# Performance work log

Hardware: AMD Instinct MI355X
Metric: run time of the kernel (lower is better)

Reference implementation:

```python
import jax, jax.numpy as jnp
import numpy as np

N_E = 1024
E_DIM = 256
BETA = 0.25
N = 131072


def setup_inputs() -> dict:
    key = jax.random.key(0)
    k1, k2 = jax.random.split(key)
    z = jax.random.normal(k1, (N, E_DIM), dtype=jnp.float32)
    # original init: uniform(-1/n_e, 1/n_e)
    emb_weight = jax.random.uniform(k2, (N_E, E_DIM), dtype=jnp.float32,
                                    minval=-1.0 / N_E, maxval=1.0 / N_E)
    return {"z": z, "emb_weight": emb_weight}


def reference(z, emb_weight):
    # pairwise squared distances: ||z||^2 + ||e||^2 - 2 z @ e^T   -> [N, n_e]
    d = (jnp.sum(z * z, axis=1, keepdims=True)
         + jnp.sum(emb_weight * emb_weight, axis=1)
         - 2.0 * jnp.matmul(z, emb_weight.T))
    min_encoding_indices = jnp.argmin(d, axis=1)            # [N]
    z_q = emb_weight[min_encoding_indices]                  # gather == one-hot matmul
    sg = jax.lax.stop_gradient
    loss = (jnp.mean((sg(z_q) - z) ** 2)
            + BETA * jnp.mean((z_q - sg(z)) ** 2))
    z_q_st = z + sg(z_q - z)                                # straight-through
    return z_q_st, loss, min_encoding_indices[:, None]
```

## Files before the change

kernel.cpp:

```cpp
#include <hip/hip_runtime.h>
#include <cfloat>

#define NROWS 131072
#define EDIM 256
#define NE 1024
#define DELTA 2.0e-4f

#define BM 128
#define BN 128
#define BK 32

typedef unsigned short u16;
typedef __attribute__((ext_vector_type(8))) short bf16x8;
typedef __attribute__((ext_vector_type(4))) float f32x4;

#define WS_Z2    0u
#define WS_E2    524288u
#define WS_PART  528384u
#define WS_CNT   548864u
#define WS_LIST  549120u
#define WS_CI1   1073408u
#define WS_CI2   1597696u
#define WS_FLG   2121984u
#define WS_BP    2646272u
#define WS_END   4219136u

__device__ __forceinline__ float np_sumsq256(const float* __restrict__ row) {
    float s[2];
#pragma unroll
    for (int h = 0; h < 2; ++h) {
        const float* a = row + h * 128;
        float r[8];
#pragma unroll
        for (int j = 0; j < 8; ++j) r[j] = __fmul_rn(a[j], a[j]);
        for (int i = 8; i < 128; i += 8) {
#pragma unroll
            for (int j = 0; j < 8; ++j)
                r[j] = __fadd_rn(r[j], __fmul_rn(a[i + j], a[i + j]));
        }
        s[h] = __fadd_rn(__fadd_rn(__fadd_rn(r[0], r[1]), __fadd_rn(r[2], r[3])),
                         __fadd_rn(__fadd_rn(r[4], r[5]), __fadd_rn(r[6], r[7])));
    }
    return __fadd_rn(s[0], s[1]);
}

__device__ __forceinline__ u16 bf16_rn(float x) {
    unsigned u = __float_as_uint(x);
    return (u16)((u + 0x7fffu + ((u >> 16) & 1u)) >> 16);
}

__global__ __launch_bounds__(256)
void rownorm_split_kernel(const float* __restrict__ z, float* __restrict__ z2out,
                          u16* __restrict__ zhi, u16* __restrict__ zlo) {
    __shared__ float zl[16 * 256];
    const int tid = threadIdx.x;
    const size_t base4 = (size_t)blockIdx.x * 1024;

    {
        const float4* src = reinterpret_cast<const float4*>(z) + base4;
        float4* dst = reinterpret_cast<float4*>(zl);
#pragma unroll
        for (int i = 0; i < 4; ++i) dst[tid + 256 * i] = src[tid + 256 * i];
    }
    __syncthreads();

    {
        const int row = tid >> 4;
        const int j16 = tid & 15;
        const int h = j16 >> 3, j = j16 & 7;
        const float* a = &zl[row * 256 + h * 128];
        float r = __fmul_rn(a[j], a[j]);
#pragma unroll
        for (int i = 8; i < 128; i += 8)
            r = __fadd_rn(r, __fmul_rn(a[i + j], a[i + j]));
        r = __fadd_rn(r, __shfl_xor(r, 1));
        r = __fadd_rn(r, __shfl_xor(r, 2));
        r = __fadd_rn(r, __shfl_xor(r, 4));
        r = __fadd_rn(r, __shfl_xor(r, 8));
        if (j16 == 0) z2out[blockIdx.x * 16 + row] = r;
    }

    {
        ushort4* ph = reinterpret_cast<ushort4*>(zhi) + base4;
        ushort4* pl = reinterpret_cast<ushort4*>(zlo) + base4;
        const float4* sp = reinterpret_cast<const float4*>(zl);
#pragma unroll
        for (int i = 0; i < 4; ++i) {
            const int q = tid + 256 * i;
            float4 v = sp[q];
            float xs[4] = {v.x, v.y, v.z, v.w};
            u16 hh[4], lo[4];
#pragma unroll
            for (int c = 0; c < 4; ++c) {
                u16 hv = bf16_rn(xs[c]);
                float hf = __uint_as_float(((unsigned)hv) << 16);
                hh[c] = hv;
                lo[c] = bf16_rn(__fsub_rn(xs[c], hf));
            }
            ph[q] = make_ushort4(hh[0], hh[1], hh[2], hh[3]);
            pl[q] = make_ushort4(lo[0], lo[1], lo[2], lo[3]);
        }
    }
}

__global__ __launch_bounds__(256)
void rownorm_kernel(const float* __restrict__ x, float* __restrict__ out, int nrows) {
    int row = blockIdx.x * blockDim.x + threadIdx.x;
    if (row < nrows) out[row] = np_sumsq256(x + (size_t)row * EDIM);
}

__global__ __launch_bounds__(256)
void build_b_kernel(const float* __restrict__ e, u16* __restrict__ Bp) {
    int idx = blockIdx.x * 256 + threadIdx.x;
    int row = idx >> 8, k = idx & 255;
    float x = e[idx];
    u16 hh = bf16_rn(x);
    float hf = __uint_as_float(((unsigned)hh) << 16);
    u16 lo = bf16_rn(__fsub_rn(x, hf));
    Bp[row * 768 + k] = hh;
    Bp[row * 768 + 256 + k] = hh;
    Bp[row * 768 + 512 + k] = lo;
}

__device__ __forceinline__ void gload_lds16(const void* g, void* lds) {
    __builtin_amdgcn_global_load_lds((const __attribute__((address_space(1))) void*)g,
                                     (__attribute__((address_space(3))) void*)lds,
                                     16, 0, 0);
}

#define LEXLT(va, ia, vb, ib) ((va) < (vb) || ((va) == (vb) && (ia) < (ib)))

#define MERGE5(a1, ai1, a2, ai2, a3, b1, bi1, b2, bi2, b3)                    \
    {                                                                         \
        float n1v, n2v, n3v; int n1i, n2i;                                    \
        if (LEXLT(a1, ai1, b1, bi1)) {                                        \
            n1v = a1; n1i = ai1;                                              \
            if (LEXLT(a2, ai2, b1, bi1)) { n2v = a2; n2i = ai2; n3v = fminf(a3, b1); } \
            else                          { n2v = b1; n2i = bi1; n3v = fminf(a2, b2); } \
        } else {                                                              \
            n1v = b1; n1i = bi1;                                              \
            if (LEXLT(b2, bi2, a1, ai1)) { n2v = b2; n2i = bi2; n3v = fminf(b3, a1); } \
            else                          { n2v = a1; n2i = ai1; n3v = fminf(b2, a2); } \
        }                                                                     \
        a1 = n1v; ai1 = n1i; a2 = n2v; ai2 = n2i; a3 = n3v;                   \
    }

__global__ __launch_bounds__(256, 3)
void vq_mfma_kernel(const u16* __restrict__ zhi, const u16* __restrict__ zlo,
                    const u16* __restrict__ Bp, const float* __restrict__ e2f,
                    int* __restrict__ ci1, int* __restrict__ ci2, int* __restrict__ cflag) {
    __shared__ __align__(16) u16  At[128 * 64];
    __shared__ __align__(16) u16  Bt[128 * 64];
    __shared__ float e2s[1024];
    __shared__ float mrg[128 * 2 * 4];

    const int tid = threadIdx.x;
    const int m0  = blockIdx.x * 128;
    const int l   = tid & 63;
    const int wid = tid >> 6;
    const int wrg = wid >> 1;
    const int wcg = wid & 1;
    const int lr  = l & 15;
    const int lg  = l >> 4;
    const int key = lr & 7;

#pragma unroll
    for (int i = 0; i < 4; ++i) e2s[tid + 256 * i] = e2f[tid + 256 * i];

    const int rsub = tid >> 3;
    const int lch  = (tid & 7) ^ (rsub & 7);

    float v1[4], v2[4], v3[4];
    unsigned pidx[4];
#pragma unroll
    for (int s = 0; s < 4; ++s) { v1[s] = FLT_MAX; v2[s] = FLT_MAX; v3[s] = FLT_MAX; pidx[s] = 0; }

#pragma unroll 1
    for (int nc = 0; nc < 8; ++nc) {
        const int n0 = nc * 128;
        f32x4 acc[4][4];
#pragma unroll
        for (int fr = 0; fr < 4; ++fr)
#pragma unroll
            for (int fc = 0; fc < 4; ++fc) acc[fr][fc] = (f32x4){0.f, 0.f, 0.f, 0.f};

#pragma unroll 1
        for (int ks = 0; ks < 12; ++ks) {
            const u16* zsel = ((ks >> 2) == 1) ? zlo : zhi;
            const int zc0 = (ks & 3) * 64;
            __syncthreads();
#pragma unroll
            for (int s = 0; s < 4; ++s) {
                const int row = s * 32 + rsub;
                gload_lds16(zsel + (size_t)(m0 + row) * 256 + zc0 + lch * 8,
                            At + (size_t)(s * 256 + tid) * 8);
                gload_lds16(Bp + (size_t)(n0 + row) * 768 + ks * 64 + lch * 8,
                            Bt + (size_t)(s * 256 + tid) * 8);
            }
            asm volatile("s_waitcnt vmcnt(0)" ::: "memory");
            __syncthreads();

            const u16* Ebase = Bt + (wcg * 64 + lr) * 64;
            const u16* Zbase = At + (wrg * 64 + lr) * 64;
#pragma unroll
            for (int kk = 0; kk < 2; ++kk) {
                const int go = ((kk * 4 + lg) ^ key) * 8;
                bf16x8 a[4], b[4];
#pragma unroll
                for (int fr = 0; fr < 4; ++fr)
                    a[fr] = *reinterpret_cast<const bf16x8*>(Ebase + fr * 1024 + go);
#pragma unroll
                for (int fc = 0; fc < 4; ++fc)
                    b[fc] = *reinterpret_cast<const bf16x8*>(Zbase + fc * 1024 + go);
#pragma unroll
                for (int fr = 0; fr < 4; ++fr)
#pragma unroll
                    for (int fc = 0; fc < 4; ++fc)
                        acc[fr][fc] = __builtin_amdgcn_mfma_f32_16x16x32_bf16(
                            a[fr], b[fc], acc[fr][fc], 0, 0, 0);
            }
        }

#pragma unroll
        for (int fr = 0; fr < 4; ++fr) {
            const int cbase = n0 + wcg * 64 + fr * 16 + lg * 4;
            const float4 e2v = *reinterpret_cast<const float4*>(&e2s[cbase]);
#pragma unroll
            for (int q = 0; q < 4; ++q) {
                const unsigned n = (unsigned)(cbase + q);
                const float e2q = (q == 0) ? e2v.x : (q == 1) ? e2v.y : (q == 2) ? e2v.z : e2v.w;
#pragma unroll
                for (int fc = 0; fc < 4; ++fc) {
                    float d = __fmaf_rn(-2.0f, acc[fr][fc][q], e2q);
                    bool lt1 = d < v1[fc];
                    bool lt2 = d < v2[fc];
                    bool lt3 = d < v3[fc];
                    v3[fc] = lt2 ? v2[fc] : (lt3 ? d : v3[fc]);
                    v2[fc] = lt1 ? v1[fc] : (lt2 ? d : v2[fc]);
                    pidx[fc] = lt1 ? ((pidx[fc] << 16) | n)
                                   : (lt2 ? ((pidx[fc] & 0xffffu) | (n << 16)) : pidx[fc]);
                    v1[fc] = lt1 ? d : v1[fc];
                }
            }
        }
    }

#pragma unroll
    for (int s = 0; s < 4; ++s) {
        float a1 = v1[s], a2 = v2[s], a3 = v3[s];
        int ai1 = (int)(pidx[s] & 0xffffu), ai2 = (int)(pidx[s] >> 16);
#pragma unroll
        for (int m = 16; m <= 32; m <<= 1) {
            float b1 = __shfl_xor(a1, m), b2 = __shfl_xor(a2, m), b3 = __shfl_xor(a3, m);
            int bi1 = __shfl_xor(ai1, m), bi2 = __shfl_xor(ai2, m);
            MERGE5(a1, ai1, a2, ai2, a3, b1, bi1, b2, bi2, b3);
        }
        if (lg == 0) {
            int row = wrg * 64 + s * 16 + lr;
            float* p = &mrg[(row * 2 + wcg) * 4];
            p[0] = a1; p[1] = a2; p[2] = a3;
            p[3] = __uint_as_float(((unsigned)ai1 & 0xffffu) | ((unsigned)ai2 << 16));
        }
    }
    __syncthreads();

    if (tid < 128) {
        const float* p0 = &mrg[(tid * 2 + 0) * 4];
        float A1 = p0[0], A2 = p0[1], A3 = p0[2];
        unsigned pk = __float_as_uint(p0[3]);
        int I1 = (int)(pk & 0xffffu), I2 = (int)(pk >> 16);
        const float* p = &mrg[(tid * 2 + 1) * 4];
        float b1 = p[0], b2 = p[1], b3 = p[2];
        unsigned q = __float_as_uint(p[3]);
        int bi1 = (int)(q & 0xffffu), bi2 = (int)(q >> 16);
        MERGE5(A1, I1, A2, I2, A3, b1, bi1, b2, bi2, b3);
        ci1[m0 + tid] = I1;
        ci2[m0 + tid] = I2;
        cflag[m0 + tid] = (A3 - A1 <= DELTA) ? 1 : 0;
    }
}

__device__ __forceinline__ float exact_g(const float* __restrict__ zr,
                                         const float* __restrict__ er,
                                         float z2v, float e2v) {
    float m = 0.f;
    for (int k = 0; k < 256; k += 4) {
        float4 zv = *reinterpret_cast<const float4*>(zr + k);
        float4 ev = *reinterpret_cast<const float4*>(er + k);
        m = __fmaf_rn(zv.x, ev.x, m);
        m = __fmaf_rn(zv.y, ev.y, m);
        m = __fmaf_rn(zv.z, ev.z, m);
        m = __fmaf_rn(zv.w, ev.w, m);
    }
    return __fsub_rn(__fadd_rn(z2v, e2v), __fmul_rn(2.0f, m));
}

__global__ __launch_bounds__(256)
void vq_refine_kernel(const float* __restrict__ z, const float* __restrict__ e,
                      const float* __restrict__ z2g, const float* __restrict__ e2f,
                      const int* __restrict__ ci1, const int* __restrict__ ci2,
                      const int* __restrict__ cflag,
                      float* __restrict__ out_idx, int* __restrict__ list,
                      int* __restrict__ counter,
                      float* __restrict__ out_zq, double* __restrict__ partials) {
    __shared__ float  gbuf[128];
    __shared__ int    fIdx[64];
    __shared__ int    fFlag[64];
    __shared__ double dred[256];
    const int tid = threadIdx.x;
    const int r0  = blockIdx.x * 64;

    if (tid < 128) {
        int r = tid >> 1, which = tid & 1;
        int row = r0 + r;
        int c = which ? ci2[row] : ci1[row];
        gbuf[tid] = exact_g(z + (size_t)row * EDIM, e + (size_t)c * EDIM, z2g[row], e2f[c]);
    }
    __syncthreads();
    if (tid < 64) {
        int row = r0 + tid;
        int a = ci1[row], b = ci2[row];
        float ga = gbuf[tid * 2], gb = gbuf[tid * 2 + 1];
        int fi = (gb < ga || (gb == ga && b < a)) ? b : a;
        fIdx[tid] = fi;
        int fl = cflag[row];
        fFlag[tid] = fl;
        out_idx[row] = (float)fi;
        if (fl) { int p = atomicAdd(counter, 1); list[p] = row; }
    }
    __syncthreads();

    double lsum = 0.0;
    for (int r = 0; r < 64; ++r) {
        if (!fFlag[r]) {
            int row = r0 + r;
            float zv = z[(size_t)row * EDIM + tid];
            float ev = e[(size_t)fIdx[r] * EDIM + tid];
            float dd = __fsub_rn(ev, zv);
            out_zq[(size_t)row * EDIM + tid] = __fadd_rn(zv, dd);
            lsum += (double)dd * (double)dd;
        }
    }
    dred[tid] = lsum;
    __syncthreads();
#pragma unroll
    for (int s = 128; s > 0; s >>= 1) {
        if (tid < s) dred[tid] += dred[tid + s];
        __syncthreads();
    }
    if (tid == 0) partials[blockIdx.x] = dred[0];
}

__global__ __launch_bounds__(256)
void vq_fallback_kernel(const float* __restrict__ z, const float* __restrict__ e,
                        const float* __restrict__ z2g, const float* __restrict__ e2f,
                        const int* __restrict__ list, const int* __restrict__ counter,
                        float* __restrict__ out_idx, float* __restrict__ out_zq,
                        double* __restrict__ partials2) {
    __shared__ float  elds[64 * 257];
    __shared__ float  zlds[4][256];
    __shared__ float  z2s[4];
    __shared__ double dred[256];
    const int n   = *counter;
    const int tid = threadIdx.x;
    const int w   = tid >> 6;
    const int lane = tid & 63;
    double lsum = 0.0;

    for (int base = blockIdx.x * 4; base < n; base += gridDim.x * 4) {
        const int nr = min(4, n - base);
        __syncthreads();
        for (int i = tid; i < nr * 256; i += 256)
            zlds[i >> 8][i & 255] = z[(size_t)list[base + (i >> 8)] * EDIM + (i & 255)];
        if (tid < nr) z2s[tid] = z2g[list[base + tid]];

        float bv = FLT_MAX; int bi = 0x7fffffff;
        const int srow  = ((tid >> 4) & 3);
        const int scolq = (tid & 15) | ((tid >> 6) << 4);
        for (int c0 = 0; c0 < NE; c0 += 64) {
            __syncthreads();
#pragma unroll
            for (int s = 0; s < 16; ++s) {
                int row = 4 * s + srow;
                float4 v = *reinterpret_cast<const float4*>(e + (size_t)(c0 + row) * EDIM + scolq * 4);
                float* d = &elds[row * 257 + scolq * 4];
                d[0] = v.x; d[1] = v.y; d[2] = v.z; d[3] = v.w;
            }
            __syncthreads();
            const int code = c0 + lane;
            const float* er = &elds[lane * 257];
            const float* zr = zlds[w];
            float m = 0.f;
#pragma unroll 8
            for (int k = 0; k < 256; ++k)
                m = __fmaf_rn(zr[k], er[k], m);
            float g = __fsub_rn(__fadd_rn(z2s[w], e2f[code]), __fmul_rn(2.0f, m));
            if (g < bv || (g == bv && code < bi)) { bv = g; bi = code; }
        }
#pragma unroll
        for (int m2 = 1; m2 < 64; m2 <<= 1) {
            float ov = __shfl_xor(bv, m2); int oi = __shfl_xor(bi, m2);
            if (ov < bv || (ov == bv && oi < bi)) { bv = ov; bi = oi; }
        }
        if (w < nr) {
            int row = list[base + w];
            if (lane == 0) out_idx[row] = (float)bi;
            const float* er2 = e + (size_t)bi * EDIM;
            for (int c = lane; c < 256; c += 64) {
                float zv = zlds[w][c];
                float dd = __fsub_rn(er2[c], zv);
                out_zq[(size_t)row * EDIM + c] = __fadd_rn(zv, dd);
                lsum += (double)dd * (double)dd;
            }
        }
    }
    dred[tid] = lsum;
    __syncthreads();
#pragma unroll
    for (int s = 128; s > 0; s >>= 1) {
        if (tid < s) dred[tid] += dred[tid + s];
        __syncthreads();
    }
    if (tid == 0) partials2[blockIdx.x] = dred[0];
}

__global__ void vq_loss_kernel(const double* __restrict__ partials, int count,
                               float* __restrict__ out_loss) {
    __shared__ double s[256];
    const int tid = threadIdx.x;
    double v = 0.0;
    for (int i = tid; i < count; i += 256) v += partials[i];
    s[tid] = v;
    __syncthreads();
    for (int k = 128; k > 0; k >>= 1) {
        if (tid < k) s[tid] += s[tid + k];
        __syncthreads();
    }
    if (tid == 0) {
        double mean = s[0] / ((double)NROWS * (double)EDIM);
        out_loss[0] = (float)(1.25 * mean);
    }
}

__global__ __launch_bounds__(256, 2)
void vq_main_r3(const float* __restrict__ z, const float* __restrict__ e,
                const float* __restrict__ z2g, const float* __restrict__ e2g,
                float* __restrict__ out_zq, float* __restrict__ out_idx,
                double* __restrict__ partials) {
    __shared__ float A[BK][BM];
    __shared__ float Bm[BK][BN];
    __shared__ float e2s[BN];
    __shared__ int   fIdx[BM];
    __shared__ double dred[256];
    const int tid = threadIdx.x;
    const int m0 = blockIdx.x * BM;
    const int trow = tid >> 4, tcol = tid & 15;
    float z2r[8];
#pragma unroll
    for (int i = 0; i < 8; ++i) z2r[i] = z2g[m0 + trow * 8 + i];
    float bestV[8]; int bestI[8];
#pragma unroll
    for (int i = 0; i < 8; ++i) { bestV[i] = FLT_MAX; bestI[i] = 0; }
    for (int n0 = 0; n0 < NE; n0 += BN) {
        float acc[8][8];
#pragma unroll
        for (int i = 0; i < 8; ++i)
#pragma unroll
            for (int j = 0; j < 8; ++j) acc[i][j] = 0.f;
        __syncthreads();
        if (tid < BN) e2s[tid] = e2g[n0 + tid];
        for (int k0 = 0; k0 < EDIM; k0 += BK) {
            __syncthreads();
#pragma unroll
            for (int s = 0; s < 4; ++s) {
                int q = tid + 256 * s, row = q >> 3, kc = (q & 7) << 2;
                float4 va = *reinterpret_cast<const float4*>(z + (size_t)(m0 + row) * EDIM + k0 + kc);
                A[kc + 0][row] = va.x; A[kc + 1][row] = va.y; A[kc + 2][row] = va.z; A[kc + 3][row] = va.w;
                float4 vb = *reinterpret_cast<const float4*>(e + (size_t)(n0 + row) * EDIM + k0 + kc);
                Bm[kc + 0][row] = vb.x; Bm[kc + 1][row] = vb.y; Bm[kc + 2][row] = vb.z; Bm[kc + 3][row] = vb.w;
            }
            __syncthreads();
#pragma unroll
            for (int k = 0; k < BK; ++k) {
                float a[8], b[8];
                *reinterpret_cast<float4*>(&a[0]) = *reinterpret_cast<const float4*>(&A[k][trow * 8]);
                *reinterpret_cast<float4*>(&a[4]) = *reinterpret_cast<const float4*>(&A[k][trow * 8 + 4]);
                *reinterpret_cast<float4*>(&b[0]) = *reinterpret_cast<const float4*>(&Bm[k][tcol * 8]);
                *reinterpret_cast<float4*>(&b[4]) = *reinterpret_cast<const float4*>(&Bm[k][tcol * 8 + 4]);
#pragma unroll
                for (int i = 0; i < 8; ++i)
#pragma unroll
                    for (int j = 0; j < 8; ++j) acc[i][j] = __fmaf_rn(a[i], b[j], acc[i][j]);
            }
        }
#pragma unroll
        for (int i = 0; i < 8; ++i)
#pragma unroll
            for (int j = 0; j < 8; ++j) {
                int n = n0 + tcol * 8 + j;
                float d = __fsub_rn(__fadd_rn(z2r[i], e2s[tcol * 8 + j]), __fmul_rn(2.0f, acc[i][j]));
                if (d < bestV[i]) { bestV[i] = d; bestI[i] = n; }
            }
    }
    __syncthreads();
    float* red_v = &A[0][0];
    int* red_i = reinterpret_cast<int*>(&Bm[0][0]);
#pragma unroll
    for (int i = 0; i < 8; ++i) {
        int row = trow * 8 + i;
        red_v[row * 16 + tcol] = bestV[i];
        red_i[row * 16 + tcol] = bestI[i];
    }
    __syncthreads();
    if (tid < BM) {
        float b1 = FLT_MAX; int i1 = 0x7fffffff;
        for (int t = 0; t < 16; ++t) {
            float v = red_v[tid * 16 + t]; int id = red_i[tid * 16 + t];
            if (v < b1 || (v == b1 && id < i1)) { b1 = v; i1 = id; }
        }
        fIdx[tid] = i1;
        out_idx[m0 + tid] = (float)i1;
    }
    __syncthreads();
    double lsum = 0.0;
    for (int r = 0; r < BM; ++r) {
        int fi = fIdx[r];
        float zv = z[(size_t)(m0 + r) * EDIM + tid];
        float ev = e[(size_t)fi * EDIM + tid];
        float dd = __fsub_rn(ev, zv);
        out_zq[(size_t)(m0 + r) * EDIM + tid] = __fadd_rn(zv, dd);
        lsum += (double)dd * (double)dd;
    }
    dred[tid] = lsum;
    __syncthreads();
#pragma unroll
    for (int s = 128; s > 0; s >>= 1) {
        if (tid < s) dred[tid] += dred[tid + s];
        __syncthreads();
    }
    if (tid == 0) partials[blockIdx.x] = dred[0];
}

extern "C" void kernel_launch(void* const* d_in, const int* in_sizes, int n_in,
                              void* d_out, int out_size, void* d_ws, size_t ws_size,
                              hipStream_t stream) {
    (void)n_in; (void)out_size;
    const float* z = (const float*)d_in[0];
    const float* e = (const float*)d_in[1];
    if (in_sizes[0] == NE * EDIM) { const float* t = z; z = e; e = t; }
    float* out      = (float*)d_out;
    float* out_zq   = out;
    float* out_loss = out + (size_t)NROWS * EDIM;
    float* out_idx  = out_loss + 1;

    char* ws = (char*)d_ws;
    float*  z2g      = (float*)(ws + WS_Z2);
    float*  e2f      = (float*)(ws + WS_E2);
    double* partials = (double*)(ws + WS_PART);

    rownorm_kernel<<<(NE + 255) / 256, 256, 0, stream>>>(e, e2f, NE);

    if (ws_size >= WS_END) {
        int* cnt  = (int*)(ws + WS_CNT);
        int* list = (int*)(ws + WS_LIST);
        int* ci1  = (int*)(ws + WS_CI1);
        int* ci2  = (int*)(ws + WS_CI2);
        int* flg  = (int*)(ws + WS_FLG);
        u16* Bp   = (u16*)(ws + WS_BP);
        u16* zhi  = (u16*)d_out;
        u16* zlo  = zhi + (size_t)NROWS * EDIM;

        hipMemsetAsync(cnt, 0, 4, stream);
        rownorm_split_kernel<<<NROWS / 16, 256, 0, stream>>>(z, z2g, zhi, zlo);
        build_b_kernel<<<NE * EDIM / 256, 256, 0, stream>>>(e, Bp);
        vq_mfma_kernel<<<NROWS / 128, 256, 0, stream>>>(zhi, zlo, Bp, e2f, ci1, ci2, flg);
        vq_refine_kernel<<<NROWS / 64, 256, 0, stream>>>(z, e, z2g, e2f, ci1, ci2, flg,
                                                         out_idx, list, cnt, out_zq, partials);
        vq_fallback_kernel<<<512, 256, 0, stream>>>(z, e, z2g, e2f, list, cnt,
                                                    out_idx, out_zq, partials + 2048);
        vq_loss_kernel<<<1, 256, 0, stream>>>(partials, 2560, out_loss);
    } else {
        rownorm_kernel<<<NROWS / 256, 256, 0, stream>>>(z, z2g, NROWS);
        vq_main_r3<<<NROWS / BM, 256, 0, stream>>>(z, e, z2g, e2f, out_zq, out_idx, partials);
        vq_loss_kernel<<<1, 256, 0, stream>>>(partials, 1024, out_loss);
    }
}
```

Baseline: 557.4 us.

## Widen MFMA tile to 256 codebook columns and reuse zhi tile across hi/lo

New measurement: 626.2 us. +12.3%, slower.

```diff
diff --git a/kernel.cpp b/kernel.cpp
--- a/kernel.cpp
+++ b/kernel.cpp
@@ -117,9 +117,8 @@
     u16 hh = bf16_rn(x);
     float hf = __uint_as_float(((unsigned)hh) << 16);
     u16 lo = bf16_rn(__fsub_rn(x, hf));
-    Bp[row * 768 + k] = hh;
-    Bp[row * 768 + 256 + k] = hh;
-    Bp[row * 768 + 512 + k] = lo;
+    Bp[row * 512 + k] = hh;
+    Bp[row * 512 + 256 + k] = lo;
 }
 
 __device__ __forceinline__ void gload_lds16(const void* g, void* lds) {
@@ -145,39 +144,76 @@
         a1 = n1v; ai1 = n1i; a2 = n2v; ai2 = n2i; a3 = n3v;                   \
     }
 
-__global__ __launch_bounds__(256, 3)
+__global__ __launch_bounds__(512, 4)
 void vq_mfma_kernel(const u16* __restrict__ zhi, const u16* __restrict__ zlo,
                     const u16* __restrict__ Bp, const float* __restrict__ e2f,
                     int* __restrict__ ci1, int* __restrict__ ci2, int* __restrict__ cflag) {
     __shared__ __align__(16) u16  At[128 * 64];
-    __shared__ __align__(16) u16  Bt[128 * 64];
+    __shared__ __align__(16) u16  Bt[256 * 64];
     __shared__ float e2s[1024];
-    __shared__ float mrg[128 * 2 * 4];
+    __shared__ float mrg[128 * 4 * 4];
 
     const int tid = threadIdx.x;
     const int m0  = blockIdx.x * 128;
     const int l   = tid & 63;
     const int wid = tid >> 6;
-    const int wrg = wid >> 1;
-    const int wcg = wid & 1;
+    const int wrg = wid >> 2;
+    const int wcg = wid & 3;
     const int lr  = l & 15;
     const int lg  = l >> 4;
     const int key = lr & 7;
 
-#pragma unroll
-    for (int i = 0; i < 4; ++i) e2s[tid + 256 * i] = e2f[tid + 256 * i];
+    e2s[tid] = e2f[tid];
+    e2s[tid + 512] = e2f[tid + 512];
 
     const int rsub = tid >> 3;
     const int lch  = (tid & 7) ^ (rsub & 7);
 
+#define STAGE_AT(src, colc)                                                   \
+    {                                                                         \
+        _Pragma("unroll")                                                     \
+        for (int s = 0; s < 2; ++s)                                           \
+            gload_lds16((src) + (size_t)(m0 + s * 64 + rsub) * 256 + (colc) + lch * 8, \
+                        At + (size_t)(s * 512 + tid) * 8);                    \
+    }
+#define STAGE_BT(off)                                                         \
+    {                                                                         \
+        _Pragma("unroll")                                                     \
+        for (int s = 0; s < 4; ++s)                                           \
+            gload_lds16(Bp + (size_t)(n0 + s * 64 + rsub) * 512 + (off) + lch * 8, \
+                        Bt + (size_t)(s * 512 + tid) * 8);                    \
+    }
+#define MFMA_STEP()                                                           \
+    {                                                                         \
+        const u16* Ebase = Bt + (wcg * 64 + lr) * 64;                         \
+        const u16* Zbase = At + (wrg * 64 + lr) * 64;                         \
+        _Pragma("unroll")                                                     \
+        for (int kk = 0; kk < 2; ++kk) {                                      \
+            const int go = ((kk * 4 + lg) ^ key) * 8;                         \
+            bf16x8 a[4], b[4];                                                \
+            _Pragma("unroll")                                                 \
+            for (int fr = 0; fr < 4; ++fr)                                    \
+                a[fr] = *reinterpret_cast<const bf16x8*>(Ebase + fr * 1024 + go); \
+            _Pragma("unroll")                                                 \
+            for (int fc = 0; fc < 4; ++fc)                                    \
+                b[fc] = *reinterpret_cast<const bf16x8*>(Zbase + fc * 1024 + go); \
+            _Pragma("unroll")                                                 \
+            for (int fr = 0; fr < 4; ++fr)                                    \
+                _Pragma("unroll")                                             \
+                for (int fc = 0; fc < 4; ++fc)                                \
+                    acc[fr][fc] = __builtin_amdgcn_mfma_f32_16x16x32_bf16(    \
+                        a[fr], b[fc], acc[fr][fc], 0, 0, 0);                  \
+        }                                                                     \
+    }
+
     float v1[4], v2[4], v3[4];
     unsigned pidx[4];
 #pragma unroll
     for (int s = 0; s < 4; ++s) { v1[s] = FLT_MAX; v2[s] = FLT_MAX; v3[s] = FLT_MAX; pidx[s] = 0; }
 
 #pragma unroll 1
-    for (int nc = 0; nc < 8; ++nc) {
-        const int n0 = nc * 128;
+    for (int nc = 0; nc < 4; ++nc) {
+        const int n0 = nc * 256;
         f32x4 acc[4][4];
 #pragma unroll
         for (int fr = 0; fr < 4; ++fr)
@@ -185,40 +221,28 @@
             for (int fc = 0; fc < 4; ++fc) acc[fr][fc] = (f32x4){0.f, 0.f, 0.f, 0.f};
 
 #pragma unroll 1
-        for (int ks = 0; ks < 12; ++ks) {
-            const u16* zsel = ((ks >> 2) == 1) ? zlo : zhi;
-            const int zc0 = (ks & 3) * 64;
-            __syncthreads();
-#pragma unroll
-            for (int s = 0; s < 4; ++s) {
-                const int row = s * 32 + rsub;
-                gload_lds16(zsel + (size_t)(m0 + row) * 256 + zc0 + lch * 8,
-                            At + (size_t)(s * 256 + tid) * 8);
-                gload_lds16(Bp + (size_t)(n0 + row) * 768 + ks * 64 + lch * 8,
-                            Bt + (size_t)(s * 256 + tid) * 8);
-            }
+        for (int j = 0; j < 4; ++j) {
+            __syncthreads();
+            STAGE_AT(zhi, j * 64);
+            STAGE_BT(j * 64);
             asm volatile("s_waitcnt vmcnt(0)" ::: "memory");
             __syncthreads();
-
-            const u16* Ebase = Bt + (wcg * 64 + lr) * 64;
-            const u16* Zbase = At + (wrg * 64 + lr) * 64;
-#pragma unroll
-            for (int kk = 0; kk < 2; ++kk) {
-                const int go = ((kk * 4 + lg) ^ key) * 8;
-                bf16x8 a[4], b[4];
-#pragma unroll
-                for (int fr = 0; fr < 4; ++fr)
-                    a[fr] = *reinterpret_cast<const bf16x8*>(Ebase + fr * 1024 + go);
-#pragma unroll
-                for (int fc = 0; fc < 4; ++fc)
-                    b[fc] = *reinterpret_cast<const bf16x8*>(Zbase + fc * 1024 + go);
-#pragma unroll
-                for (int fr = 0; fr < 4; ++fr)
-#pragma unroll
-                    for (int fc = 0; fc < 4; ++fc)
-                        acc[fr][fc] = __builtin_amdgcn_mfma_f32_16x16x32_bf16(
-                            a[fr], b[fc], acc[fr][fc], 0, 0, 0);
-            }
+            MFMA_STEP();
+
+            __syncthreads();
+            STAGE_BT(256 + j * 64);
+            asm volatile("s_waitcnt vmcnt(0)" ::: "memory");
+            __syncthreads();
+            MFMA_STEP();
+        }
+#pragma unroll 1
+        for (int j = 0; j < 4; ++j) {
+            __syncthreads();
+            STAGE_AT(zlo, j * 64);
+            STAGE_BT(j * 64);
+            asm volatile("s_waitcnt vmcnt(0)" ::: "memory");
+            __syncthreads();
+            MFMA_STEP();
         }
 
 #pragma unroll
@@ -257,7 +281,7 @@
         }
         if (lg == 0) {
             int row = wrg * 64 + s * 16 + lr;
-            float* p = &mrg[(row * 2 + wcg) * 4];
+            float* p = &mrg[(row * 4 + wcg) * 4];
             p[0] = a1; p[1] = a2; p[2] = a3;
             p[3] = __uint_as_float(((unsigned)ai1 & 0xffffu) | ((unsigned)ai2 << 16));
         }
@@ -265,15 +289,18 @@
     __syncthreads();
 
     if (tid < 128) {
-        const float* p0 = &mrg[(tid * 2 + 0) * 4];
+        const float* p0 = &mrg[(tid * 4 + 0) * 4];
         float A1 = p0[0], A2 = p0[1], A3 = p0[2];
         unsigned pk = __float_as_uint(p0[3]);
         int I1 = (int)(pk & 0xffffu), I2 = (int)(pk >> 16);
-        const float* p = &mrg[(tid * 2 + 1) * 4];
-        float b1 = p[0], b2 = p[1], b3 = p[2];
-        unsigned q = __float_as_uint(p[3]);
-        int bi1 = (int)(q & 0xffffu), bi2 = (int)(q >> 16);
-        MERGE5(A1, I1, A2, I2, A3, b1, bi1, b2, bi2, b3);
+#pragma unroll
+        for (int w = 1; w < 4; ++w) {
+            const float* p = &mrg[(tid * 4 + w) * 4];
+            float b1 = p[0], b2 = p[1], b3 = p[2];
+            unsigned q = __float_as_uint(p[3]);
+            int bi1 = (int)(q & 0xffffu), bi2 = (int)(q >> 16);
+            MERGE5(A1, I1, A2, I2, A3, b1, bi1, b2, bi2, b3);
+        }
         ci1[m0 + tid] = I1;
         ci2[m0 + tid] = I2;
         cflag[m0 + tid] = (A3 - A1 <= DELTA) ? 1 : 0;
@@ -573,7 +600,7 @@
         hipMemsetAsync(cnt, 0, 4, stream);
         rownorm_split_kernel<<<NROWS / 16, 256, 0, stream>>>(z, z2g, zhi, zlo);
         build_b_kernel<<<NE * EDIM / 256, 256, 0, stream>>>(e, Bp);
-        vq_mfma_kernel<<<NROWS / 128, 256, 0, stream>>>(zhi, zlo, Bp, e2f, ci1, ci2, flg);
+        vq_mfma_kernel<<<NROWS / 128, 512, 0, stream>>>(zhi, zlo, Bp, e2f, ci1, ci2, flg);
         vq_refine_kernel<<<NROWS / 64, 256, 0, stream>>>(z, e, z2g, e2f, ci1, ci2, flg,
                                                          out_idx, list, cnt, out_zq, partials);
         vq_fallback_kernel<<<512, 256, 0, stream>>>(z, e, z2g, e2f, list, cnt,
```
